# Kernel tuning notes

Measured on AMD Instinct MI355X. Metric: run time of the kernel, lower is better.

Reference implementation:

```python
import jax, jax.numpy as jnp
import numpy as np


def setup_inputs() -> dict:
    key = jax.random.key(0)
    k1, k2 = jax.random.split(key)
    B, L, D = 16, 1024, 256
    sentence1 = jax.random.normal(k1, (B, L, D), dtype=jnp.float32)
    sentence2 = jax.random.normal(k2, (B, L, D), dtype=jnp.float32)
    return {"batch_size": B, "sentence1": sentence1, "sentence2": sentence2}


def reference(batch_size, sentence1, sentence2):
    # A[k,i,j] = 1 / (1 + ||s1[k,i] - s2[k,j]||_2)
    # materializing the [B, L1, L2, D] difference tensor.
    x2 = jnp.sum(sentence1 * sentence1, axis=-1)          # [B, L1]
    y2 = jnp.sum(sentence2 * sentence2, axis=-1)          # [B, L2]
    xy = jnp.einsum("bid,bjd->bij", sentence1, sentence2)  # [B, L1, L2]
    sq = x2[:, :, None] + y2[:, None, :] - 2.0 * xy
    sq = jnp.maximum(sq, 0.0)  # guard tiny negatives from cancellation
    dist = jnp.sqrt(sq)
    return 1.0 / (1.0 + dist)
```

## Files before the change

kernel.cpp:

```cpp
#include <hip/hip_runtime.h>
#include <hip/hip_bf16.h>

typedef __attribute__((ext_vector_type(4))) float f32x4;
typedef __attribute__((ext_vector_type(8))) __bf16 bf16x8;
typedef __attribute__((ext_vector_type(4))) __bf16 bf16x4;

#define B_DIM 16
#define L_DIM 1024
#define D_DIM 256

#define GLOAD_LDS16(g, lptr)                                          \
    __builtin_amdgcn_global_load_lds(                                 \
        (const __attribute__((address_space(1))) void*)(g),           \
        (__attribute__((address_space(3))) void*)(lptr), 16, 0, 0)

__global__ __launch_bounds__(256) void prep_kernel(const float* __restrict__ s1,
                                                   const float* __restrict__ s2,
                                                   float* __restrict__ nrm,
                                                   __hip_bfloat16* __restrict__ s1b,
                                                   __hip_bfloat16* __restrict__ s2b) {
    const int w = threadIdx.x >> 6, l = threadIdx.x & 63;
    const int base = (blockIdx.x << 4) + (w << 2);
#pragma unroll
    for (int i = 0; i < 4; ++i) {
        const int row = base + i;
        const int second = row >> 14;
        const int r = row & 16383;
        const float* src = (second ? s2 : s1) + (size_t)r * D_DIM;
        __hip_bfloat16* dst = (second ? s2b : s1b) + (size_t)r * D_DIM;
        float4 v = reinterpret_cast<const float4*>(src)[l];
        float s = v.x * v.x + v.y * v.y + v.z * v.z + v.w * v.w;
        bf16x4 bv;
        bv[0] = (__bf16)v.x; bv[1] = (__bf16)v.y; bv[2] = (__bf16)v.z; bv[3] = (__bf16)v.w;
        *reinterpret_cast<bf16x4*>(dst + l * 4) = bv;
#pragma unroll
        for (int o = 32; o > 0; o >>= 1) s += __shfl_xor(s, o, 64);
        if (l == 0) nrm[row] = s;
    }
}

__global__ __launch_bounds__(256) void dist_gemm_bf16_kernel(const __hip_bfloat16* __restrict__ s1b,
                                                             const __hip_bfloat16* __restrict__ s2b,
                                                             const float* __restrict__ nrm,
                                                             float* __restrict__ out) {
    __shared__ __bf16 Alds[4][128 * 32];
    __shared__ __bf16 Blds[4][128 * 32];

    const int t = threadIdx.x;
    const int p = blockIdx.x;
    const int d = ((p & 7) << 7) + (p >> 3);
    const int batch = d >> 6;
    const int tile = d & 63;
    const int row0 = (tile >> 3) << 7;
    const int col0 = (tile & 7) << 7;

    const __hip_bfloat16* Ag = s1b + ((size_t)batch * L_DIM + row0) * D_DIM;
    const __hip_bfloat16* Bg = s2b + ((size_t)batch * L_DIM + col0) * D_DIM;

    const int l = t & 63, w = t >> 6;
    const int wr = w >> 1, wc = w & 1;
    const int lr = l & 15;
    const int lq = l >> 4;

    const int srow_in_seg = l >> 2;
    const int sslot = (l & 3) ^ ((l >> 3) & 3);

    f32x4 acc[4][4] = {};

    auto stageK = [&](int kt) {
        const int k0 = kt << 5;
        const int b = kt & 3;
#pragma unroll
        for (int i = 0; i < 2; ++i) {
            const int s = (w << 1) | i;
            const int rl = (s << 4) + srow_in_seg;
            GLOAD_LDS16(Ag + rl * D_DIM + k0 + sslot * 8, &Alds[b][s << 9]);
            GLOAD_LDS16(Bg + rl * D_DIM + k0 + sslot * 8, &Blds[b][s << 9]);
        }
    };

    auto readFrags = [&](int kt, bf16x8* aF, bf16x8* bF) {
        const int b = kt & 3;
#pragma unroll
        for (int m = 0; m < 4; ++m) {
            const int row = (wr << 6) + (m << 4) + lr;
            const int sl = lq ^ ((row >> 1) & 3);
            aF[m] = *reinterpret_cast<const bf16x8*>(&Alds[b][(row << 5) + (sl << 3)]);
        }
#pragma unroll
        for (int n = 0; n < 4; ++n) {
            const int row = (wc << 6) + (n << 4) + lr;
            const int sl = lq ^ ((row >> 1) & 3);
            bF[n] = *reinterpret_cast<const bf16x8*>(&Blds[b][(row << 5) + (sl << 3)]);
        }
    };

    bf16x8 aF[2][4], bF[2][4];

    stageK(0); stageK(1); stageK(2);
    asm volatile("s_waitcnt vmcnt(4)" ::: "memory");
    __builtin_amdgcn_s_barrier();
    readFrags(0, aF[0], bF[0]);

#pragma unroll
    for (int kt = 0; kt < 8; ++kt) {
        if (kt >= 1) {
            if (kt <= 5) asm volatile("s_waitcnt vmcnt(4)" ::: "memory");
            else         asm volatile("s_waitcnt vmcnt(0)" ::: "memory");
            __builtin_amdgcn_s_barrier();
        }
        if (kt < 7) readFrags(kt + 1, aF[(kt + 1) & 1], bF[(kt + 1) & 1]);
        if (kt < 7) asm volatile("s_waitcnt lgkmcnt(8)" ::: "memory");
        else        asm volatile("s_waitcnt lgkmcnt(0)" ::: "memory");
        if (kt <= 4) stageK(kt + 3);

        __builtin_amdgcn_s_setprio(1);
#pragma unroll
        for (int m = 0; m < 4; ++m)
#pragma unroll
            for (int n = 0; n < 4; ++n)
                acc[m][n] = __builtin_amdgcn_mfma_f32_16x16x32_bf16(
                    aF[kt & 1][m], bF[kt & 1][n], acc[m][n], 0, 0, 0);
        __builtin_amdgcn_s_setprio(0);
    }

    const float* x2 = nrm + batch * L_DIM;
    const float* y2 = nrm + B_DIM * L_DIM + batch * L_DIM;
    float* outb = out + (size_t)batch * L_DIM * L_DIM;
    const int rbase = row0 + (wr << 6) + (lq << 2);
    const int cbase = col0 + (wc << 6) + lr;
#pragma unroll
    for (int n = 0; n < 4; ++n) {
        const int col = cbase + (n << 4);
        const float y2v = y2[col];
#pragma unroll
        for (int m = 0; m < 4; ++m) {
            const int rowf = rbase + (m << 4);
#pragma unroll
            for (int r = 0; r < 4; ++r) {
                const int row = rowf + r;
                float sq = x2[row] + y2v - 2.0f * acc[m][n][r];
                sq = fmaxf(sq, 0.0f);
                float den = 1.0f + __builtin_amdgcn_sqrtf(sq);
                outb[(size_t)row * L_DIM + col] = __builtin_amdgcn_rcpf(den);
            }
        }
    }
}

__global__ __launch_bounds__(256) void norms_kernel(const float* __restrict__ s1,
                                                    const float* __restrict__ s2,
                                                    float* __restrict__ nrm) {
    int w = threadIdx.x >> 6, l = threadIdx.x & 63;
    int row = (blockIdx.x << 2) + w;
    const float* src = (row < B_DIM * L_DIM)
                           ? (s1 + (size_t)row * D_DIM)
                           : (s2 + (size_t)(row - B_DIM * L_DIM) * D_DIM);
    float4 v = reinterpret_cast<const float4*>(src)[l];
    float s = v.x * v.x + v.y * v.y + v.z * v.z + v.w * v.w;
#pragma unroll
    for (int o = 32; o > 0; o >>= 1) s += __shfl_xor(s, o, 64);
    if (l == 0) nrm[row] = s;
}

__global__ __launch_bounds__(256) void dist_gemm_kernel(const float* __restrict__ s1,
                                                        const float* __restrict__ s2,
                                                        const float* __restrict__ nrm,
                                                        float* __restrict__ out) {
    __shared__ __bf16 Alds[2][128 * 32];
    __shared__ __bf16 Blds[2][128 * 32];

    const int t = threadIdx.x;
    const int p = blockIdx.x;
    const int d = ((p & 7) << 7) + (p >> 3);
    const int batch = d >> 6;
    const int tile = d & 63;
    const int row0 = (tile >> 3) << 7;
    const int col0 = (tile & 7) << 7;

    const float* Ag = s1 + ((size_t)batch * L_DIM + row0) * D_DIM;
    const float* Bg = s2 + ((size_t)batch * L_DIM + col0) * D_DIM;

    const int sr = t >> 2;
    const int sc = (t & 3) << 3;

    const int l = t & 63, w = t >> 6;
    const int wr = w >> 1, wc = w & 1;
    const int lr = l & 15;
    const int lk = (l >> 4) << 3;

    f32x4 acc[4][4] = {};

    auto stage = [&](int buf, int k0) {
#pragma unroll
        for (int pass = 0; pass < 2; ++pass) {
            const int r = sr + (pass << 6);
            const float4* sa = reinterpret_cast<const float4*>(Ag + (size_t)r * D_DIM + k0 + sc);
            float4 a0 = sa[0], a1 = sa[1];
            const float4* sb = reinterpret_cast<const float4*>(Bg + (size_t)r * D_DIM + k0 + sc);
            float4 b0 = sb[0], b1 = sb[1];
            bf16x8 av, bv;
            av[0] = (__bf16)a0.x; av[1] = (__bf16)a0.y; av[2] = (__bf16)a0.z; av[3] = (__bf16)a0.w;
            av[4] = (__bf16)a1.x; av[5] = (__bf16)a1.y; av[6] = (__bf16)a1.z; av[7] = (__bf16)a1.w;
            bv[0] = (__bf16)b0.x; bv[1] = (__bf16)b0.y; bv[2] = (__bf16)b0.z; bv[3] = (__bf16)b0.w;
            bv[4] = (__bf16)b1.x; bv[5] = (__bf16)b1.y; bv[6] = (__bf16)b1.z; bv[7] = (__bf16)b1.w;
            *reinterpret_cast<bf16x8*>(&Alds[buf][(r << 5) + sc]) = av;
            *reinterpret_cast<bf16x8*>(&Blds[buf][(r << 5) + sc]) = bv;
        }
    };

    stage(0, 0);
    __syncthreads();
    int cur = 0;
    for (int kt = 0; kt < 8; ++kt) {
        if (kt < 7) stage(cur ^ 1, (kt + 1) << 5);
        bf16x8 aF[4], bF[4];
#pragma unroll
        for (int m = 0; m < 4; ++m)
            aF[m] = *reinterpret_cast<const bf16x8*>(
                &Alds[cur][(((wr << 6) + (m << 4) + lr) << 5) + lk]);
#pragma unroll
        for (int n = 0; n < 4; ++n)
            bF[n] = *reinterpret_cast<const bf16x8*>(
                &Blds[cur][(((wc << 6) + (n << 4) + lr) << 5) + lk]);
#pragma unroll
        for (int m = 0; m < 4; ++m)
#pragma unroll
            for (int n = 0; n < 4; ++n)
                acc[m][n] = __builtin_amdgcn_mfma_f32_16x16x32_bf16(aF[m], bF[n], acc[m][n], 0, 0, 0);
        __syncthreads();
        cur ^= 1;
    }

    const float* x2 = nrm + batch * L_DIM;
    const float* y2 = nrm + B_DIM * L_DIM + batch * L_DIM;
    float* outb = out + (size_t)batch * L_DIM * L_DIM;
    const int rbase = row0 + (wr << 6) + ((l >> 4) << 2);
    const int cbase = col0 + (wc << 6) + lr;
#pragma unroll
    for (int n = 0; n < 4; ++n) {
        const int col = cbase + (n << 4);
        const float y2v = y2[col];
#pragma unroll
        for (int m = 0; m < 4; ++m) {
            const int rowf = rbase + (m << 4);
#pragma unroll
            for (int r = 0; r < 4; ++r) {
                const int row = rowf + r;
                float sq = x2[row] + y2v - 2.0f * acc[m][n][r];
                sq = fmaxf(sq, 0.0f);
                outb[(size_t)row * L_DIM + col] = 1.0f / (1.0f + sqrtf(sq));
            }
        }
    }
}

extern "C" void kernel_launch(void* const* d_in, const int* in_sizes, int n_in,
                              void* d_out, int out_size, void* d_ws, size_t ws_size,
                              hipStream_t stream) {
    (void)in_sizes; (void)n_in; (void)out_size;
    const float* s1 = (const float*)d_in[1];
    const float* s2 = (const float*)d_in[2];
    float* out = (float*)d_out;

    const size_t NRM_BYTES = 2u * B_DIM * L_DIM * sizeof(float);
    const size_t BF_BYTES = (size_t)B_DIM * L_DIM * D_DIM * sizeof(__hip_bfloat16);
    const size_t NEED = NRM_BYTES + 2 * BF_BYTES;

    float* nrm = (float*)d_ws;
    if (ws_size >= NEED) {
        __hip_bfloat16* s1b = (__hip_bfloat16*)((char*)d_ws + NRM_BYTES);
        __hip_bfloat16* s2b = (__hip_bfloat16*)((char*)d_ws + NRM_BYTES + BF_BYTES);
        prep_kernel<<<2048, 256, 0, stream>>>(s1, s2, nrm, s1b, s2b);
        dist_gemm_bf16_kernel<<<1024, 256, 0, stream>>>(s1b, s2b, nrm, out);
    } else {
        norms_kernel<<<8192, 256, 0, stream>>>(s1, s2, nrm);
        dist_gemm_kernel<<<1024, 256, 0, stream>>>(s1, s2, nrm, out);
    }
}
```

Measured before the change: 34.58 us.

## Process two output tiles per block, overlapping first epilogue with second prefetch

Each workgroup now computes two adjacent 128x128 output tiles in sequence, and the grid is halved to 512 blocks. The second tile's first K stages are issued before the first tile's epilogue runs, so global loads overlap the distance math and the large output stores. The norm values are preloaded early, and vmcnt thresholds are adjusted to account for the extra in-flight loads and stores. This costs higher register pressure from the two accumulator sets, fewer blocks to spread over the CUs, and fragile hand-tuned waitcnt values.

```diff
diff --git a/kernel.cpp b/kernel.cpp
--- a/kernel.cpp
+++ b/kernel.cpp
@@ -13,6 +13,8 @@
     __builtin_amdgcn_global_load_lds(                                 \
         (const __attribute__((address_space(1))) void*)(g),           \
         (__attribute__((address_space(3))) void*)(lptr), 16, 0, 0)
+
+#define SBAR() __builtin_amdgcn_sched_barrier(0)
 
 __global__ __launch_bounds__(256) void prep_kernel(const float* __restrict__ s1,
                                                    const float* __restrict__ s2,
@@ -39,23 +41,25 @@
     }
 }
 
-__global__ __launch_bounds__(256) void dist_gemm_bf16_kernel(const __hip_bfloat16* __restrict__ s1b,
-                                                             const __hip_bfloat16* __restrict__ s2b,
-                                                             const float* __restrict__ nrm,
-                                                             float* __restrict__ out) {
+__global__ __launch_bounds__(256, 2) void dist_gemm2_kernel(const __hip_bfloat16* __restrict__ s1b,
+                                                            const __hip_bfloat16* __restrict__ s2b,
+                                                            const float* __restrict__ nrm,
+                                                            float* __restrict__ out) {
     __shared__ __bf16 Alds[4][128 * 32];
     __shared__ __bf16 Blds[4][128 * 32];
 
     const int t = threadIdx.x;
     const int p = blockIdx.x;
-    const int d = ((p & 7) << 7) + (p >> 3);
-    const int batch = d >> 6;
-    const int tile = d & 63;
-    const int row0 = (tile >> 3) << 7;
-    const int col0 = (tile & 7) << 7;
+    const int d = ((p & 7) << 6) + (p >> 3);
+    const int batch = d >> 5;
+    const int rem = d & 31;
+    const int row0 = (rem >> 2) << 7;
+    const int col0a = (rem & 3) << 8;
+    const int col0b = col0a + 128;
 
     const __hip_bfloat16* Ag = s1b + ((size_t)batch * L_DIM + row0) * D_DIM;
-    const __hip_bfloat16* Bg = s2b + ((size_t)batch * L_DIM + col0) * D_DIM;
+    const __hip_bfloat16* Bg0 = s2b + ((size_t)batch * L_DIM + col0a) * D_DIM;
+    const __hip_bfloat16* Bg1 = s2b + ((size_t)batch * L_DIM + col0b) * D_DIM;
 
     const int l = t & 63, w = t >> 6;
     const int wr = w >> 1, wc = w & 1;
@@ -65,9 +69,7 @@
     const int srow_in_seg = l >> 2;
     const int sslot = (l & 3) ^ ((l >> 3) & 3);
 
-    f32x4 acc[4][4] = {};
-
-    auto stageK = [&](int kt) {
+    auto stageK = [&](const __hip_bfloat16* Bg, int kt) {
         const int k0 = kt << 5;
         const int b = kt & 3;
 #pragma unroll
@@ -79,73 +81,118 @@
         }
     };
 
-    auto readFrags = [&](int kt, bf16x8* aF, bf16x8* bF) {
+    bf16x8 aF[2][4], bF[2][4];
+    auto readFrags = [&](int kt, bf16x8* a, bf16x8* bfr) {
         const int b = kt & 3;
 #pragma unroll
         for (int m = 0; m < 4; ++m) {
             const int row = (wr << 6) + (m << 4) + lr;
             const int sl = lq ^ ((row >> 1) & 3);
-            aF[m] = *reinterpret_cast<const bf16x8*>(&Alds[b][(row << 5) + (sl << 3)]);
+            a[m] = *reinterpret_cast<const bf16x8*>(&Alds[b][(row << 5) + (sl << 3)]);
         }
 #pragma unroll
         for (int n = 0; n < 4; ++n) {
             const int row = (wc << 6) + (n << 4) + lr;
             const int sl = lq ^ ((row >> 1) & 3);
-            bF[n] = *reinterpret_cast<const bf16x8*>(&Blds[b][(row << 5) + (sl << 3)]);
+            bfr[n] = *reinterpret_cast<const bf16x8*>(&Blds[b][(row << 5) + (sl << 3)]);
         }
     };
 
-    bf16x8 aF[2][4], bF[2][4];
-
-    stageK(0); stageK(1); stageK(2);
-    asm volatile("s_waitcnt vmcnt(4)" ::: "memory");
+    const float* x2 = nrm + batch * L_DIM;
+    const float* y2 = nrm + B_DIM * L_DIM + batch * L_DIM;
+    const int rbase = row0 + (wr << 6) + (lq << 2);
+    const int cloc = (wc << 6) + lr;
+
+    float* outb = out + (size_t)batch * L_DIM * L_DIM;
+    auto epilogue = [&](const f32x4 (&acc)[4][4], const f32x4 (&xv)[4],
+                        const float (&yv)[4], int col0_) {
+        const int cb = col0_ + cloc;
+#pragma unroll
+        for (int n = 0; n < 4; ++n) {
+            const int col = cb + (n << 4);
+            const float y2v = yv[n];
+#pragma unroll
+            for (int m = 0; m < 4; ++m) {
+#pragma unroll
+                for (int r = 0; r < 4; ++r) {
+                    const int row = rbase + (m << 4) + r;
+                    float sq = xv[m][r] + y2v - 2.0f * acc[m][n][r];
+                    sq = fmaxf(sq, 0.0f);
+                    float den = 1.0f + __builtin_amdgcn_sqrtf(sq);
+                    outb[(size_t)row * L_DIM + col] = __builtin_amdgcn_rcpf(den);
+                }
+            }
+        }
+    };
+
+    f32x4 acc0[4][4] = {};
+    stageK(Bg0, 0); stageK(Bg0, 1); stageK(Bg0, 2);
+    SBAR();
+    f32x4 xv[4]; float yv0[4];
+#pragma unroll
+    for (int m = 0; m < 4; ++m) xv[m] = *reinterpret_cast<const f32x4*>(&x2[rbase + (m << 4)]);
+#pragma unroll
+    for (int n = 0; n < 4; ++n) yv0[n] = y2[col0a + cloc + (n << 4)];
+    SBAR();
+    asm volatile("s_waitcnt vmcnt(12)" ::: "memory");
     __builtin_amdgcn_s_barrier();
     readFrags(0, aF[0], bF[0]);
 
 #pragma unroll
     for (int kt = 0; kt < 8; ++kt) {
-        if (kt >= 1) {
-            if (kt <= 5) asm volatile("s_waitcnt vmcnt(4)" ::: "memory");
-            else         asm volatile("s_waitcnt vmcnt(0)" ::: "memory");
-            __builtin_amdgcn_s_barrier();
-        }
+        if (kt == 1)      asm volatile("s_waitcnt vmcnt(12)" ::: "memory");
+        else if (kt >= 2 && kt <= 5) asm volatile("s_waitcnt vmcnt(4)" ::: "memory");
+        else if (kt >= 6) asm volatile("s_waitcnt vmcnt(0)" ::: "memory");
+        if (kt >= 1) __builtin_amdgcn_s_barrier();
         if (kt < 7) readFrags(kt + 1, aF[(kt + 1) & 1], bF[(kt + 1) & 1]);
         if (kt < 7) asm volatile("s_waitcnt lgkmcnt(8)" ::: "memory");
         else        asm volatile("s_waitcnt lgkmcnt(0)" ::: "memory");
-        if (kt <= 4) stageK(kt + 3);
-
+        if (kt <= 4) stageK(Bg0, kt + 3);
         __builtin_amdgcn_s_setprio(1);
 #pragma unroll
         for (int m = 0; m < 4; ++m)
 #pragma unroll
             for (int n = 0; n < 4; ++n)
-                acc[m][n] = __builtin_amdgcn_mfma_f32_16x16x32_bf16(
-                    aF[kt & 1][m], bF[kt & 1][n], acc[m][n], 0, 0, 0);
+                acc0[m][n] = __builtin_amdgcn_mfma_f32_16x16x32_bf16(
+                    aF[kt & 1][m], bF[kt & 1][n], acc0[m][n], 0, 0, 0);
         __builtin_amdgcn_s_setprio(0);
     }
 
-    const float* x2 = nrm + batch * L_DIM;
-    const float* y2 = nrm + B_DIM * L_DIM + batch * L_DIM;
-    float* outb = out + (size_t)batch * L_DIM * L_DIM;
-    const int rbase = row0 + (wr << 6) + (lq << 2);
-    const int cbase = col0 + (wc << 6) + lr;
-#pragma unroll
-    for (int n = 0; n < 4; ++n) {
-        const int col = cbase + (n << 4);
-        const float y2v = y2[col];
-#pragma unroll
-        for (int m = 0; m < 4; ++m) {
-            const int rowf = rbase + (m << 4);
-#pragma unroll
-            for (int r = 0; r < 4; ++r) {
-                const int row = rowf + r;
-                float sq = x2[row] + y2v - 2.0f * acc[m][n][r];
-                sq = fmaxf(sq, 0.0f);
-                float den = 1.0f + __builtin_amdgcn_sqrtf(sq);
-                outb[(size_t)row * L_DIM + col] = __builtin_amdgcn_rcpf(den);
-            }
-        }
-    }
+    stageK(Bg1, 0); stageK(Bg1, 1); stageK(Bg1, 2);
+    SBAR();
+    float yv1[4];
+#pragma unroll
+    for (int n = 0; n < 4; ++n) yv1[n] = y2[col0b + cloc + (n << 4)];
+    SBAR();
+    epilogue(acc0, xv, yv0, col0a);
+    SBAR();
+    asm volatile("s_waitcnt vmcnt(24)" ::: "memory");
+    __builtin_amdgcn_s_barrier();
+
+    f32x4 acc1[4][4] = {};
+    readFrags(0, aF[0], bF[0]);
+
+#pragma unroll
+    for (int kt = 0; kt < 8; ++kt) {
+        if (kt == 1)      asm volatile("s_waitcnt vmcnt(24)" ::: "memory");
+        else if (kt >= 2 && kt <= 5) asm volatile("s_waitcnt vmcnt(4)" ::: "memory");
+        else if (kt >= 6) asm volatile("s_waitcnt vmcnt(0)" ::: "memory");
+        if (kt >= 1) __builtin_amdgcn_s_barrier();
+        if (kt < 7) readFrags(kt + 1, aF[(kt + 1) & 1], bF[(kt + 1) & 1]);
+        if (kt < 7) asm volatile("s_waitcnt lgkmcnt(8)" ::: "memory");
+        else        asm volatile("s_waitcnt lgkmcnt(0)" ::: "memory");
+        if (kt <= 4) stageK(Bg1, kt + 3);
+        __builtin_amdgcn_s_setprio(1);
+#pragma unroll
+        for (int m = 0; m < 4; ++m)
+#pragma unroll
+            for (int n = 0; n < 4; ++n)
+                acc1[m][n] = __builtin_amdgcn_mfma_f32_16x16x32_bf16(
+                    aF[kt & 1][m], bF[kt & 1][n], acc1[m][n], 0, 0, 0);
+        __builtin_amdgcn_s_setprio(0);
+    }
+
+    epilogue(acc1, xv, yv1, col0b);
 }
 
 __global__ __launch_bounds__(256) void norms_kernel(const float* __restrict__ s1,
@@ -272,7 +319,7 @@
         __hip_bfloat16* s1b = (__hip_bfloat16*)((char*)d_ws + NRM_BYTES);
         __hip_bfloat16* s2b = (__hip_bfloat16*)((char*)d_ws + NRM_BYTES + BF_BYTES);
         prep_kernel<<<2048, 256, 0, stream>>>(s1, s2, nrm, s1b, s2b);
-        dist_gemm_bf16_kernel<<<1024, 256, 0, stream>>>(s1b, s2b, nrm, out);
+        dist_gemm2_kernel<<<512, 256, 0, stream>>>(s1b, s2b, nrm, out);
     } else {
         norms_kernel<<<8192, 256, 0, stream>>>(s1, s2, nrm);
         dist_gemm_kernel<<<1024, 256, 0, stream>>>(s1, s2, nrm, out);
```

Result: faster. 32.17 us (-7.0%).
